# Kernel optimization log

Hardware: AMD Instinct MI355X
Metric: run time of the kernel (lower is better)

Reference implementation:

```python
import jax, jax.numpy as jnp
import numpy as np

N = 50000
DIN, DH, DOUT = 128, 128, 64
DEPTH = 3
TEMP = 1.0
WEIGHT = 0.5
LN_EPS = 1e-5
E_RAND = 1_600_000


def setup_inputs() -> dict:
    key = jax.random.key(0)
    ks = jax.random.split(key, 16)
    x = jax.random.normal(ks[0], (N, DIN), jnp.float32)
    # random edges + ring (guarantees degree >= 2 after symmetrization)
    src = jax.random.randint(ks[1], (E_RAND,), 0, N)
    dst = jax.random.randint(ks[2], (E_RAND,), 0, N)
    ring = jnp.arange(N)
    s = jnp.concatenate([src, ring])
    d = jnp.concatenate([dst, (ring + 1) % N])
    edge_index = jnp.stack([jnp.concatenate([s, d]), jnp.concatenate([d, s])]).astype(jnp.int64)  # [2, 3.3M], symmetric

    def glorot(k, i, o):
        return jax.random.normal(k, (i, o), jnp.float32) * jnp.sqrt(2.0 / (i + o)).astype(jnp.float32)

    return {
        "x": x, "edge_index": edge_index,
        "W0": glorot(ks[3], DIN, DH), "b0": jnp.zeros((DH,), jnp.float32),
        "W1": glorot(ks[4], DH, DH),  "b1": jnp.zeros((DH,), jnp.float32),
        "W2": glorot(ks[5], DH, DH),  "b2": jnp.zeros((DH,), jnp.float32),
        "W_out": glorot(ks[6], DH, DOUT), "b_out": jnp.zeros((DOUT,), jnp.float32),
        "gamma": jnp.ones((DH,), jnp.float32), "beta": jnp.zeros((DH,), jnp.float32),
    }


def _seg(vals, idx):
    return jax.ops.segment_sum(vals, idx, num_segments=N)


def _gcn_conv(h_in, W, b, src, dst):
    # PyG GCNConv: self-loops, sym norm D^-1/2 (A+I) D^-1/2
    h = h_in @ W
    ones = jnp.ones(src.shape, jnp.float32)
    deg = _seg(ones, dst) + 1.0  # degree incl. self-loop
    dinv = jax.lax.rsqrt(deg)
    msg = h[src] * (dinv[src] * dinv[dst])[:, None]
    return _seg(msg, dst) + h * (1.0 / deg)[:, None] + b


def _layernorm(x, g, b):
    m = jnp.mean(x, axis=-1, keepdims=True)
    v = jnp.mean((x - m) ** 2, axis=-1, keepdims=True)
    return (x - m) * jax.lax.rsqrt(v + LN_EPS) * g + b


def reference(x, edge_index, W0, b0, W1, b1, W2, b2, W_out, b_out, gamma, beta):
    src, dst = edge_index[0], edge_index[1]
    h = x
    for W, b in ((W0, b0), (W1, b1), (W2, b2)):
        h = _layernorm(jax.nn.relu(_gcn_conv(h, W, b, src, dst)), gamma, beta)
    emb = _gcn_conv(h, W_out, b_out, src, dst)  # [N, DOUT]

    # --- entropy gradient (edge-list form of the dense-A einsums) ---
    ones = jnp.ones(src.shape, jnp.float32)
    deg_adj = _seg(ones, src)                     # row sums of A (no self-loops)
    en_norm = 1.0 / jnp.sqrt(deg_adj * DH)        # uses hidden_dim, as in the original

    rn2 = jnp.sum(emb * emb, axis=1)              # ||X_i||^2
    dot = jnp.sum(emb[src] * emb[dst], axis=1)    # <X_i, X_j> per edge
    res1 = deg_adj * rn2
    res2 = _seg(dot, src)
    res3 = _seg(rn2[dst], src)
    energies = 0.5 * (res1 - 2.0 * res2 + res3) * en_norm  # normalize_energies=True

    logits = -energies / TEMP
    P = jax.nn.softmax(logits, axis=0) + 1e-10
    logP = jnp.log(P)
    S = -jnp.sum(P * logP)
    Pbar = P * (S + logP)                         # [N]

    nsumX = _seg(emb[dst], src)                   # sum_j A_ij X_j
    nsumP = _seg(Pbar[dst], src)                  # sum_j A_ij Pbar_j
    XP = emb * Pbar[:, None]
    g1 = deg_adj[:, None] * XP
    g2 = emb * nsumP[:, None]
    g3 = Pbar[:, None] * nsumX
    g4 = _seg(XP[dst], src)
    grad_S = (g1 + g2 - g3 - g4) / TEMP * en_norm[:, None]

    return emb + WEIGHT * grad_S
```

## Files before the change

### kernel.cpp

```cpp
#include <hip/hip_runtime.h>
#include <hip/hip_fp16.h>

#define DIN 128
#define DH  128
#define DFO 64
#define LN_EPS 1e-5f
#define WEIGHT 0.5f

#define MAXB  104
#define CAPB  48
#define FLUSH 32
#define SENT  0xFFFFFFFFu

typedef unsigned int uint32;
typedef unsigned short ushort16;

__device__ __forceinline__ float h_lo(uint32 u) { return __half2float(__ushort_as_half((unsigned short)(u & 0xFFFFu))); }
__device__ __forceinline__ float h_hi(uint32 u) { return __half2float(__ushort_as_half((unsigned short)(u >> 16))); }
__device__ __forceinline__ uint32 pack_h2(float a, float b) {
  return (uint32)__half_as_ushort(__float2half_rn(a)) | ((uint32)__half_as_ushort(__float2half_rn(b)) << 16);
}
__device__ __forceinline__ float ub0(uint32 u) { return (float)(u & 0xffu); }
__device__ __forceinline__ float ub1(uint32 u) { return (float)((u >> 8) & 0xffu); }
__device__ __forceinline__ float ub2(uint32 u) { return (float)((u >> 16) & 0xffu); }
__device__ __forceinline__ float ub3(uint32 u) { return (float)(u >> 24); }

__device__ __forceinline__ float wave_sum(float v) {
  #pragma unroll
  for (int off = 32; off > 0; off >>= 1) v += __shfl_xor(v, off);
  return v;
}
__device__ __forceinline__ float wave_max(float v) {
  #pragma unroll
  for (int off = 32; off > 0; off >>= 1) v = fmaxf(v, __shfl_xor(v, off));
  return v;
}

__device__ __forceinline__ void fq16u(float* a, uint4 u, float w) {
  a[0]  = fmaf(ub0(u.x), w, a[0]);  a[1]  = fmaf(ub1(u.x), w, a[1]);
  a[2]  = fmaf(ub2(u.x), w, a[2]);  a[3]  = fmaf(ub3(u.x), w, a[3]);
  a[4]  = fmaf(ub0(u.y), w, a[4]);  a[5]  = fmaf(ub1(u.y), w, a[5]);
  a[6]  = fmaf(ub2(u.y), w, a[6]);  a[7]  = fmaf(ub3(u.y), w, a[7]);
  a[8]  = fmaf(ub0(u.z), w, a[8]);  a[9]  = fmaf(ub1(u.z), w, a[9]);
  a[10] = fmaf(ub2(u.z), w, a[10]); a[11] = fmaf(ub3(u.z), w, a[11]);
  a[12] = fmaf(ub0(u.w), w, a[12]); a[13] = fmaf(ub1(u.w), w, a[13]);
  a[14] = fmaf(ub2(u.w), w, a[14]); a[15] = fmaf(ub3(u.w), w, a[15]);
}

__global__ __launch_bounds__(64) void k_prep(const float* __restrict__ g, const float* __restrict__ b,
                      const float* __restrict__ W1, const float* __restrict__ W2,
                      const float* __restrict__ Wo, float* __restrict__ Wg1,
                      float* __restrict__ Wg2, float* __restrict__ Wgo,
                      float* __restrict__ vecs) {
  int c = blockIdx.x * 64 + threadIdx.x;
  const float* W; float* Wg; float* gv; float* bv; int ld; int col;
  if (c < 128)      { W = W1; Wg = Wg1; gv = vecs;       bv = vecs + 128; ld = 128; col = c; }
  else if (c < 256) { W = W2; Wg = Wg2; gv = vecs + 256; bv = vecs + 384; ld = 128; col = c - 128; }
  else              { W = Wo; Wg = Wgo; gv = vecs + 512; bv = vecs + 576; ld = 64;  col = c - 256; }
  float gs = 0.f, bs = 0.f;
  for (int k = 0; k < 128; ++k) {
    float w = W[k * ld + col];
    float gk = g[k];
    Wg[k * ld + col] = gk * w;
    gs += gk * w;
    bs += b[k] * w;
  }
  gv[col] = gs; bv[col] = bs;
}

__global__ __launch_bounds__(256) void k_bin3(const int* __restrict__ src, const int* __restrict__ dst,
                       int E2, int nbc, int GCAP, int* __restrict__ gbcnt,
                       uint32* __restrict__ gpairs) {
  __shared__ uint32 lbuf[MAXB][CAPB];
  __shared__ int lcnt[MAXB];
  __shared__ int fbase[MAXB];
  __shared__ int fm[MAXB];
  __shared__ short flist[MAXB];
  __shared__ int fn;
  int wv = threadIdx.x >> 6, ln = threadIdx.x & 63;
  for (int b = threadIdx.x; b < nbc; b += 256) lcnt[b] = 0;
  __syncthreads();

  for (int base = blockIdx.x * 256; base < E2; base += gridDim.x * 256) {
    int i = base + threadIdx.x;
    if (i < E2) {
      int s = src[i], d = dst[i];
      int b0 = s >> 9;
      uint32 v0 = ((uint32)(s & 511) << 16) | (uint32)d;
      int sl = atomicAdd(&lcnt[b0], 1);
      if (sl < CAPB) lbuf[b0][sl] = v0;
      else { int g = atomicAdd(&gbcnt[b0 * 16], 1); gpairs[(size_t)b0 * GCAP + g] = v0; }
      int b1 = d >> 9;
      uint32 v1 = ((uint32)(d & 511) << 16) | (uint32)s;
      sl = atomicAdd(&lcnt[b1], 1);
      if (sl < CAPB) lbuf[b1][sl] = v1;
      else { int g = atomicAdd(&gbcnt[b1 * 16], 1); gpairs[(size_t)b1 * GCAP + g] = v1; }
    }
    if (threadIdx.x == 0) fn = 0;
    __syncthreads();
    if (threadIdx.x < nbc) {
      int m = lcnt[threadIdx.x];
      if (m >= FLUSH) {
        if (m > CAPB) m = CAPB;
        int r = (m + 15) & ~15;
        fbase[threadIdx.x] = atomicAdd(&gbcnt[threadIdx.x * 16], r);
        fm[threadIdx.x] = m;
        int fi = atomicAdd(&fn, 1);
        flist[fi] = (short)threadIdx.x;
      }
    }
    __syncthreads();
    int nf = fn;
    for (int fi = wv; fi < nf; fi += 4) {
      int b = flist[fi];
      int m = fm[b], r = (m + 15) & ~15, g = fbase[b];
      if (ln < r)
        gpairs[(size_t)b * GCAP + g + ln] = (ln < m) ? lbuf[b][ln] : SENT;
    }
    __syncthreads();
    if (threadIdx.x < nbc && lcnt[threadIdx.x] >= FLUSH) lcnt[threadIdx.x] = 0;
    __syncthreads();
  }
  if (threadIdx.x < nbc) {
    int m = lcnt[threadIdx.x]; if (m > CAPB) m = CAPB;
    fm[threadIdx.x] = m;
    if (m > 0) {
      int r = (m + 15) & ~15;
      fbase[threadIdx.x] = atomicAdd(&gbcnt[threadIdx.x * 16], r);
    }
  }
  __syncthreads();
  for (int b = wv; b < nbc; b += 4) {
    int m = fm[b];
    if (m > 0) {
      int r = (m + 15) & ~15, g = fbase[b];
      if (ln < r)
        gpairs[(size_t)b * GCAP + g + ln] = (ln < m) ? lbuf[b][ln] : SENT;
    }
  }
}

__global__ __launch_bounds__(1024) void k_csr(const uint32* __restrict__ gpairs, const int* __restrict__ gbcnt,
                      int GCAP, int GCAPC, int N, int* __restrict__ rowbeg, int* __restrict__ rowcnt,
                      float* __restrict__ dinv, float* __restrict__ cntf, ushort16* __restrict__ col) {
  __shared__ int hist[512];
  __shared__ int pos[512];
  int b = blockIdx.x, tid = threadIdx.x;
  if (tid < 512) hist[tid] = 0;
  __syncthreads();
  int m = gbcnt[b * 16];
  const uint32* pp = gpairs + (size_t)b * GCAP;
  for (int t = tid; t < m; t += 1024) {
    uint32 v = pp[t];
    if (v != SENT) atomicAdd(&hist[v >> 16], 1);
  }
  __syncthreads();
  int cnt = (tid < 512) ? hist[tid] : 0;
  for (int off = 1; off < 512; off <<= 1) {
    int u = (tid >= off && tid < 512) ? hist[tid - off] : 0;
    __syncthreads();
    if (tid < 512) hist[tid] += u;
    __syncthreads();
  }
  int cbase = b * GCAPC;
  if (tid < 512) {
    int excl = hist[tid] - cnt;
    pos[tid] = excl;
    int node = (b << 9) + tid;
    if (node < N) {
      rowbeg[node] = cbase + excl;
      rowcnt[node] = cnt;
      cntf[node] = (float)cnt;
      dinv[node] = rsqrtf((float)cnt + 1.0f);
    }
  }
  __syncthreads();
  for (int t = tid; t < m; t += 1024) {
    uint32 v = pp[t];
    if (v != SENT) {
      int sl = atomicAdd(&pos[v >> 16], 1);
      col[cbase + sl] = (ushort16)(v & 0xFFFFu);
    }
  }
}

template <int COLS, int MODE>
__global__ __launch_bounds__(256) void k_gemm(const void* __restrict__ Ap, const float* __restrict__ W,
                            const float* __restrict__ dinv, const float2* __restrict__ stats,
                            const float* __restrict__ gW, const float* __restrict__ bW,
                            uint32* __restrict__ qout, float* __restrict__ qsc, int N) {
  const int CG  = COLS / 4;
  const int RG  = 256 / CG;
  const int RPT = 64 / RG;
  __shared__ float4 At4[64 * 32];
  int t = threadIdx.x;
  int rbase = blockIdx.x * 64;
  #pragma unroll
  for (int i2 = 0; i2 < 8; ++i2) {
    int idx = t + 256 * i2;
    int row = idx >> 5, c4i = idx & 31;
    int gr = rbase + row;
    float4 v = make_float4(0.f, 0.f, 0.f, 0.f);
    if (gr < N) {
      if (MODE == 1) {
        uint2 p = ((const uint2*)Ap)[(size_t)gr * 32 + c4i];
        v = make_float4(h_lo(p.x), h_hi(p.x), h_lo(p.y), h_hi(p.y));
      } else {
        v = ((const float4*)Ap)[(size_t)gr * 32 + c4i];
      }
    }
    At4[idx] = v;
  }
  __syncthreads();
  int c4 = t % CG, rg = t / CG;
  float acc[RPT][4];
  #pragma unroll
  for (int r = 0; r < RPT; ++r) { acc[r][0] = acc[r][1] = acc[r][2] = acc[r][3] = 0.f; }
  const float4* W4 = (const float4*)W;
  #pragma unroll 2
  for (int k4 = 0; k4 < 32; ++k4) {
    float4 w0 = W4[(k4 * 4 + 0) * CG + c4];
    float4 w1 = W4[(k4 * 4 + 1) * CG + c4];
    float4 w2 = W4[(k4 * 4 + 2) * CG + c4];
    float4 w3 = W4[(k4 * 4 + 3) * CG + c4];
    #pragma unroll
    for (int r = 0; r < RPT; ++r) {
      float4 av = At4[(rg * RPT + r) * 32 + k4];
      acc[r][0] = fmaf(av.x, w0.x, acc[r][0]); acc[r][0] = fmaf(av.y, w1.x, acc[r][0]);
      acc[r][0] = fmaf(av.z, w2.x, acc[r][0]); acc[r][0] = fmaf(av.w, w3.x, acc[r][0]);
      acc[r][1] = fmaf(av.x, w0.y, acc[r][1]); acc[r][1] = fmaf(av.y, w1.y, acc[r][1]);
      acc[r][1] = fmaf(av.z, w2.y, acc[r][1]); acc[r][1] = fmaf(av.w, w3.y, acc[r][1]);
      acc[r][2] = fmaf(av.x, w0.z, acc[r][2]); acc[r][2] = fmaf(av.y, w1.z, acc[r][2]);
      acc[r][2] = fmaf(av.z, w2.z, acc[r][2]); acc[r][2] = fmaf(av.w, w3.z, acc[r][2]);
      acc[r][3] = fmaf(av.x, w0.w, acc[r][3]); acc[r][3] = fmaf(av.y, w1.w, acc[r][3]);
      acc[r][3] = fmaf(av.z, w2.w, acc[r][3]); acc[r][3] = fmaf(av.w, w3.w, acc[r][3]);
    }
  }
  float4 g4 = make_float4(0.f, 0.f, 0.f, 0.f), b4 = make_float4(0.f, 0.f, 0.f, 0.f);
  if (MODE == 1) { g4 = ((const float4*)gW)[c4]; b4 = ((const float4*)bW)[c4]; }
  #pragma unroll
  for (int r = 0; r < RPT; ++r) {
    int gr = rbase + rg * RPT + r;
    float o0 = 0.f, o1 = 0.f, o2 = 0.f, o3 = 0.f;
    if (gr < N) {
      float s = dinv[gr];
      if (MODE == 1) {
        float2 st = stats[gr];
        o0 = s * (st.y * (acc[r][0] - st.x * g4.x) + b4.x);
        o1 = s * (st.y * (acc[r][1] - st.x * g4.y) + b4.y);
        o2 = s * (st.y * (acc[r][2] - st.x * g4.z) + b4.z);
        o3 = s * (st.y * (acc[r][3] - st.x * g4.w) + b4.w);
      } else {
        o0 = acc[r][0] * s; o1 = acc[r][1] * s; o2 = acc[r][2] * s; o3 = acc[r][3] * s;
      }
    }
    float mx = fmaxf(fmaxf(fabsf(o0), fabsf(o1)), fmaxf(fabsf(o2), fabsf(o3)));
    #pragma unroll
    for (int m = 1; m < CG; m <<= 1) mx = fmaxf(mx, __shfl_xor(mx, m));
    if (gr < N) {
      float inv = (mx > 0.f) ? 127.f / mx : 0.f;
      int q0 = (int)rintf(o0 * inv) + 128, q1 = (int)rintf(o1 * inv) + 128;
      int q2 = (int)rintf(o2 * inv) + 128, q3 = (int)rintf(o3 * inv) + 128;
      uint32 qw = (uint32)q0 | ((uint32)q1 << 8) | ((uint32)q2 << 16) | ((uint32)q3 << 24);
      qout[(size_t)gr * CG + c4] = qw;
      if (c4 == 0) qsc[gr] = mx * (1.f / 127.f);
    }
  }
}

__global__ __launch_bounds__(64) void k_aggh(const uint4* __restrict__ hq4, const float* __restrict__ hsc,
                      const int* __restrict__ rowbeg, const int* __restrict__ rowcnt,
                      const ushort16* __restrict__ col, const float* __restrict__ dinv,
                      const float* __restrict__ bias, uint4* __restrict__ vh4,
                      float2* __restrict__ stats, int N) {
  int i = blockIdx.x, lane = threadIdx.x;
  int f = lane & 7, sl = lane >> 3;
  int beg = rowbeg[i], end = beg + rowcnt[i];
  float a[16];
  #pragma unroll
  for (int k = 0; k < 16; ++k) a[k] = 0.f;
  float ssum = 0.f;
  {
    float si = hsc[i];
    if (lane < 8) fq16u(a, hq4[(size_t)i * 8 + f], si);
    if (lane == 0) ssum += si;
  }
  int t = beg + sl;
  for (; t + 8 < end; t += 16) {
    int j0 = col[t], j1 = col[t + 8];
    float s0 = hsc[j0], s1 = hsc[j1];
    uint4 u0 = hq4[(size_t)j0 * 8 + f];
    uint4 u1 = hq4[(size_t)j1 * 8 + f];
    fq16u(a, u0, s0); fq16u(a, u1, s1);
    if (f == 0) ssum += s0 + s1;
  }
  if (t < end) {
    int j = col[t];
    float s0 = hsc[j];
    fq16u(a, hq4[(size_t)j * 8 + f], s0);
    if (f == 0) ssum += s0;
  }
  #pragma unroll
  for (int k = 0; k < 16; ++k) {
    a[k] += __shfl_xor(a[k], 8);
    a[k] += __shfl_xor(a[k], 16);
    a[k] += __shfl_xor(a[k], 32);
  }
  float ssT = wave_sum(ssum) * 128.f;
  if (lane < 8) {
    float di = dinv[i];
    const float4* bb = (const float4*)bias + f * 4;
    float s = 0.f, s2 = 0.f;
    #pragma unroll
    for (int q = 0; q < 4; ++q) {
      float4 b4 = bb[q];
      float v0 = fmaxf(fmaf(a[q*4+0] - ssT, di, b4.x), 0.f);
      float v1 = fmaxf(fmaf(a[q*4+1] - ssT, di, b4.y), 0.f);
      float v2 = fmaxf(fmaf(a[q*4+2] - ssT, di, b4.z), 0.f);
      float v3 = fmaxf(fmaf(a[q*4+3] - ssT, di, b4.w), 0.f);
      a[q*4+0] = v0; a[q*4+1] = v1; a[q*4+2] = v2; a[q*4+3] = v3;
      s += (v0 + v1) + (v2 + v3);
      s2 += (v0*v0 + v1*v1) + (v2*v2 + v3*v3);
    }
    s += __shfl_xor(s, 1); s2 += __shfl_xor(s2, 1);
    s += __shfl_xor(s, 2); s2 += __shfl_xor(s2, 2);
    s += __shfl_xor(s, 4); s2 += __shfl_xor(s2, 4);
    uint4 o0, o1;
    o0.x = pack_h2(a[0], a[1]);   o0.y = pack_h2(a[2], a[3]);
    o0.z = pack_h2(a[4], a[5]);   o0.w = pack_h2(a[6], a[7]);
    o1.x = pack_h2(a[8], a[9]);   o1.y = pack_h2(a[10], a[11]);
    o1.z = pack_h2(a[12], a[13]); o1.w = pack_h2(a[14], a[15]);
    vh4[(size_t)i * 16 + f * 2]     = o0;
    vh4[(size_t)i * 16 + f * 2 + 1] = o1;
    if (lane == 0) {
      float mean = s * (1.f / 128.f);
      float var  = s2 * (1.f / 128.f) - mean * mean;
      stats[i] = make_float2(mean, rsqrtf(var + LN_EPS));
    }
  }
}

__global__ __launch_bounds__(64) void k_agg_out(const uint4* __restrict__ hq4, const float* __restrict__ hsc,
                          const int* __restrict__ rowbeg, const int* __restrict__ rowcnt,
                          const ushort16* __restrict__ col, const float* __restrict__ dinv,
                          const float* __restrict__ bias, float* __restrict__ embf,
                          uint4* __restrict__ embq4, float2* __restrict__ escr2, int N) {
  int i = blockIdx.x, lane = threadIdx.x;
  int f4 = lane & 3, sl = lane >> 2;
  int beg = rowbeg[i], end = beg + rowcnt[i];
  float a[16];
  #pragma unroll
  for (int k = 0; k < 16; ++k) a[k] = 0.f;
  float ssum = 0.f;
  {
    float si = hsc[i];
    if (lane < 4) fq16u(a, hq4[(size_t)i * 4 + f4], si);
    if (lane == 0) ssum += si;
  }
  int t = beg + sl;
  for (; t + 16 < end; t += 32) {
    int j0 = col[t], j1 = col[t + 16];
    float s0 = hsc[j0], s1 = hsc[j1];
    uint4 u0 = hq4[(size_t)j0 * 4 + f4];
    uint4 u1 = hq4[(size_t)j1 * 4 + f4];
    fq16u(a, u0, s0); fq16u(a, u1, s1);
    if (f4 == 0) ssum += s0 + s1;
  }
  if (t < end) {
    int j = col[t];
    float s0 = hsc[j];
    fq16u(a, hq4[(size_t)j * 4 + f4], s0);
    if (f4 == 0) ssum += s0;
  }
  #pragma unroll
  for (int k = 0; k < 16; ++k) {
    a[k] += __shfl_xor(a[k], 4);  a[k] += __shfl_xor(a[k], 8);
    a[k] += __shfl_xor(a[k], 16); a[k] += __shfl_xor(a[k], 32);
  }
  float ssT = wave_sum(ssum) * 128.f;
  if (lane < 4) {
    float di = dinv[i];
    const float4* bb = (const float4*)bias + f4 * 4;
    float s2 = 0.f, mx = 0.f;
    #pragma unroll
    for (int q = 0; q < 4; ++q) {
      float4 b4 = bb[q];
      float e0 = fmaf(a[q*4+0] - ssT, di, b4.x);
      float e1 = fmaf(a[q*4+1] - ssT, di, b4.y);
      float e2 = fmaf(a[q*4+2] - ssT, di, b4.z);
      float e3 = fmaf(a[q*4+3] - ssT, di, b4.w);
      a[q*4+0] = e0; a[q*4+1] = e1; a[q*4+2] = e2; a[q*4+3] = e3;
      s2 += (e0*e0 + e1*e1) + (e2*e2 + e3*e3);
      mx = fmaxf(mx, fmaxf(fmaxf(fabsf(e0), fabsf(e1)), fmaxf(fabsf(e2), fabsf(e3))));
      ((float4*)embf)[(size_t)i * 16 + f4 * 4 + q] = make_float4(e0, e1, e2, e3);
    }
    s2 += __shfl_xor(s2, 1); s2 += __shfl_xor(s2, 2);
    mx = fmaxf(mx, __shfl_xor(mx, 1)); mx = fmaxf(mx, __shfl_xor(mx, 2));
    float inv = (mx > 0.f) ? 127.f / mx : 0.f;
    uint4 qo;
    uint32* qw = (uint32*)&qo;
    #pragma unroll
    for (int q = 0; q < 4; ++q) {
      int q0 = (int)rintf(a[q*4+0] * inv) + 128, q1 = (int)rintf(a[q*4+1] * inv) + 128;
      int q2 = (int)rintf(a[q*4+2] * inv) + 128, q3 = (int)rintf(a[q*4+3] * inv) + 128;
      qw[q] = (uint32)q0 | ((uint32)q1 << 8) | ((uint32)q2 << 16) | ((uint32)q3 << 24);
    }
    embq4[(size_t)i * 4 + f4] = qo;
    if (lane == 0) escr2[i] = make_float2(mx * (1.f / 127.f), s2);
  }
}

__global__ __launch_bounds__(64) void k_passA(const float* __restrict__ embf, const uint4* __restrict__ embq4,
                        const float2* __restrict__ escr2, const int* __restrict__ rowbeg,
                        const int* __restrict__ rowcnt, const ushort16* __restrict__ col,
                        const float* __restrict__ cntf, float* __restrict__ nsumX,
                        float* __restrict__ logits, int N) {
  int i = blockIdx.x, lane = threadIdx.x;
  int f4 = lane & 3, sl = lane >> 2;
  int beg = rowbeg[i], end = beg + rowcnt[i];
  float a[16];
  #pragma unroll
  for (int k = 0; k < 16; ++k) a[k] = 0.f;
  float r3 = 0.f, escs = 0.f;
  int t = beg + sl;
  for (; t + 16 < end; t += 32) {
    int j0 = col[t], j1 = col[t + 16];
    float2 er0 = escr2[j0], er1 = escr2[j1];
    uint4 u0 = embq4[(size_t)j0 * 4 + f4];
    uint4 u1 = embq4[(size_t)j1 * 4 + f4];
    fq16u(a, u0, er0.x); fq16u(a, u1, er1.x);
    if (f4 == 0) { r3 += er0.y + er1.y; escs += er0.x + er1.x; }
  }
  if (t < end) {
    int j = col[t];
    float2 er = escr2[j];
    fq16u(a, embq4[(size_t)j * 4 + f4], er.x);
    if (f4 == 0) { r3 += er.y; escs += er.x; }
  }
  #pragma unroll
  for (int k = 0; k < 16; ++k) {
    a[k] += __shfl_xor(a[k], 4);  a[k] += __shfl_xor(a[k], 8);
    a[k] += __shfl_xor(a[k], 16); a[k] += __shfl_xor(a[k], 32);
  }
  r3 = wave_sum(r3);
  float ssT = wave_sum(escs) * 128.f;
  if (lane < 4) {
    float dd = 0.f;
    #pragma unroll
    for (int q = 0; q < 4; ++q) {
      float n0 = a[q*4+0] - ssT, n1 = a[q*4+1] - ssT;
      float n2 = a[q*4+2] - ssT, n3 = a[q*4+3] - ssT;
      float4 e = ((const float4*)embf)[(size_t)i * 16 + f4 * 4 + q];
      dd += e.x * n0 + e.y * n1 + e.z * n2 + e.w * n3;
      ((float4*)nsumX)[(size_t)i * 16 + f4 * 4 + q] = make_float4(n0, n1, n2, n3);
    }
    dd += __shfl_xor(dd, 1); dd += __shfl_xor(dd, 2);
    if (lane == 0) {
      float c = cntf[i];
      float en = rsqrtf(c * 128.0f);
      logits[i] = -0.5f * (c * escr2[i].y - 2.f * dd + r3) * en;
    }
  }
}

__global__ __launch_bounds__(256) void k_sm1(const float* __restrict__ logits, int N,
                                             float4* __restrict__ partials) {
  int idx = blockIdx.x * 256 + threadIdx.x;
  int w = threadIdx.x >> 6, ln = threadIdx.x & 63;
  float x = (idx < N) ? logits[idx] : -3.4e38f;
  float m = wave_max(x);
  __shared__ float red[3][4];
  if (ln == 0) red[0][w] = m;
  __syncthreads();
  float M = fmaxf(fmaxf(red[0][0], red[0][1]), fmaxf(red[0][2], red[0][3]));
  float ev = (idx < N) ? expf(x - M) : 0.f;
  float tv = (idx < N) ? (x - M) * ev : 0.f;
  float se = wave_sum(ev), st = wave_sum(tv);
  if (ln == 0) { red[1][w] = se; red[2][w] = st; }
  __syncthreads();
  if (threadIdx.x == 0)
    partials[blockIdx.x] = make_float4(M, red[1][0] + red[1][1] + red[1][2] + red[1][3],
                                          red[2][0] + red[2][1] + red[2][2] + red[2][3], 0.f);
}

__global__ __launch_bounds__(256) void k_sm2(const float4* __restrict__ partials, int nb,
                                             float* __restrict__ scal) {
  int tid = threadIdx.x;
  int w = tid >> 6, ln = tid & 63;
  float4 p = (tid < nb) ? partials[tid] : make_float4(-3.4e38f, 0.f, 0.f, 0.f);
  float m = wave_max(p.x);
  __shared__ float red[3][4];
  if (ln == 0) red[0][w] = m;
  __syncthreads();
  float M = fmaxf(fmaxf(red[0][0], red[0][1]), fmaxf(red[0][2], red[0][3]));
  float sc = (tid < nb) ? expf(p.x - M) : 0.f;
  float se = p.y * sc;
  float tt = (p.z + (p.x - M) * p.y) * sc;
  se = wave_sum(se); tt = wave_sum(tt);
  if (ln == 0) { red[1][w] = se; red[2][w] = tt; }
  __syncthreads();
  if (tid == 0) {
    float SE = red[1][0] + red[1][1] + red[1][2] + red[1][3];
    float TT = red[2][0] + red[2][1] + red[2][2] + red[2][3];
    scal[0] = M;
    scal[1] = SE;
    scal[2] = logf(SE) - TT / SE;
  }
}

__global__ __launch_bounds__(256) void k_pbar(const float* __restrict__ logits, int N,
                     const float* __restrict__ scal, const float2* __restrict__ escr2,
                     float2* __restrict__ pw2) {
  float M = scal[0], SE = scal[1], S = scal[2];
  int i = blockIdx.x * blockDim.x + threadIdx.x;
  int stride = gridDim.x * blockDim.x;
  for (; i < N; i += stride) {
    float p = expf(logits[i] - M) / SE + 1e-10f;
    float pb = p * (S + logf(p));
    pw2[i] = make_float2(pb, pb * escr2[i].x);
  }
}

__global__ __launch_bounds__(64) void k_passB(const float* __restrict__ embf, const uint4* __restrict__ embq4,
                        const float2* __restrict__ pw2, const int* __restrict__ rowbeg,
                        const int* __restrict__ rowcnt, const ushort16* __restrict__ col,
                        const float* __restrict__ cntf, float* __restrict__ outp, int N) {
  int i = blockIdx.x, lane = threadIdx.x;
  int f4 = lane & 3, sl = lane >> 2;
  int beg = rowbeg[i], end = beg + rowcnt[i];
  float a[16];
  #pragma unroll
  for (int k = 0; k < 16; ++k) a[k] = 0.f;
  float sp = 0.f, pys = 0.f;
  int t = beg + sl;
  for (; t + 16 < end; t += 32) {
    int j0 = col[t], j1 = col[t + 16];
    float2 p0 = pw2[j0], p1 = pw2[j1];
    uint4 u0 = embq4[(size_t)j0 * 4 + f4];
    uint4 u1 = embq4[(size_t)j1 * 4 + f4];
    fq16u(a, u0, p0.y); fq16u(a, u1, p1.y);
    if (f4 == 0) { sp += p0.x + p1.x; pys += p0.y + p1.y; }
  }
  if (t < end) {
    int j = col[t];
    float2 p = pw2[j];
    fq16u(a, embq4[(size_t)j * 4 + f4], p.y);
    if (f4 == 0) { sp += p.x; pys += p.y; }
  }
  #pragma unroll
  for (int k = 0; k < 16; ++k) {
    a[k] += __shfl_xor(a[k], 4);  a[k] += __shfl_xor(a[k], 8);
    a[k] += __shfl_xor(a[k], 16); a[k] += __shfl_xor(a[k], 32);
  }
  sp = wave_sum(sp);
  float ssT = wave_sum(pys) * 128.f;
  if (lane < 4) {
    float Pi = pw2[i].x;
    float c = cntf[i];
    float wgt = WEIGHT * rsqrtf(c * 128.0f);
    #pragma unroll
    for (int q = 0; q < 4; ++q) {
      float4 e = ((const float4*)embf)[(size_t)i * 16 + f4 * 4 + q];
      float4 n = ((const float4*)outp)[(size_t)i * 16 + f4 * 4 + q];
      float x0 = a[q*4+0] - ssT, x1 = a[q*4+1] - ssT;
      float x2 = a[q*4+2] - ssT, x3 = a[q*4+3] - ssT;
      float g0 = c * e.x * Pi + e.x * sp - Pi * n.x - x0;
      float g1 = c * e.y * Pi + e.y * sp - Pi * n.y - x1;
      float g2 = c * e.z * Pi + e.z * sp - Pi * n.z - x2;
      float g3 = c * e.w * Pi + e.w * sp - Pi * n.w - x3;
      ((float4*)outp)[(size_t)i * 16 + f4 * 4 + q] =
          make_float4(fmaf(wgt, g0, e.x), fmaf(wgt, g1, e.y), fmaf(wgt, g2, e.z), fmaf(wgt, g3, e.w));
    }
  }
}

extern "C" void kernel_launch(void* const* d_in, const int* in_sizes, int n_in,
                              void* d_out, int out_size, void* d_ws, size_t ws_size,
                              hipStream_t stream) {
  const float* x     = (const float*)d_in[0];
  const int*   ei    = (const int*)d_in[1];
  const float* W0    = (const float*)d_in[2];
  const float* b0    = (const float*)d_in[3];
  const float* W1    = (const float*)d_in[4];
  const float* b1    = (const float*)d_in[5];
  const float* W2    = (const float*)d_in[6];
  const float* b2    = (const float*)d_in[7];
  const float* Wo    = (const float*)d_in[8];
  const float* bo    = (const float*)d_in[9];
  const float* gamma = (const float*)d_in[10];
  const float* beta  = (const float*)d_in[11];

  int N = in_sizes[0] / DIN;
  int E = in_sizes[1] / 2;
  int E2 = E / 2;
  const int* src = ei;
  const int* dst = ei + E;
  int nbc = (N + 511) >> 9;
  int perb = E / nbc;
  int GCAP  = ((perb + perb / 3 + 8192) + 15) & ~15;
  int GCAPC = perb + 4096;

  char* w = (char*)d_ws;
  auto alloc = [&](size_t bytes) { void* p = w; w += (bytes + 255) & ~(size_t)255; return p; };
  char* regA = (char*)alloc((size_t)N * 128 * 2);
  char* regB = (char*)alloc((size_t)N * 128);
  char* pad  = (char*)alloc((size_t)3 * 1024 * 1024);
  (void)pad;
  ushort16* colx = (ushort16*)alloc((size_t)nbc * GCAPC * 2);
  int*    rowbeg = (int*)alloc((size_t)N * 4);
  int*    rowcnt = (int*)alloc((size_t)N * 4);
  float*  dinv   = (float*)alloc((size_t)N * 4);
  float*  cntf   = (float*)alloc((size_t)N * 4);
  float*  logits = (float*)alloc((size_t)N * 4);
  float*  hsc    = (float*)alloc((size_t)N * 4);
  float*  oscq   = (float*)alloc((size_t)N * 4);
  float2* escr2  = (float2*)alloc((size_t)N * 8);
  float2* pw2    = (float2*)alloc((size_t)N * 8);
  float2* stats  = (float2*)alloc((size_t)N * 8);
  float*  Wg1    = (float*)alloc(128 * 128 * 4);
  float*  Wg2    = (float*)alloc(128 * 128 * 4);
  float*  Wgo    = (float*)alloc(128 * 64 * 4);
  float*  vecs   = (float*)alloc(640 * 4);
  int*    gbcnt  = (int*)alloc((size_t)MAXB * 16 * 4);
  float4* partials = (float4*)alloc(4096);
  float*  scal   = (float*)alloc(256);

  uint32* gpairs = (uint32*)regA;
  uint4*  vh4    = (uint4*)regA;
  float*  embf   = (float*)regA;
  uint32* hq     = (uint32*)regB;
  uint32* hoq    = (uint32*)regB;
  uint4*  embq4  = (uint4*)(regB + (size_t)N * 64);

  hipMemsetAsync(gbcnt, 0, (size_t)MAXB * 64, stream);
  k_prep<<<5, 64, 0, stream>>>(gamma, beta, W1, W2, Wo, Wg1, Wg2, Wgo, vecs);
  k_bin3<<<1024, 256, 0, stream>>>(src, dst, E2, nbc, GCAP, gbcnt, gpairs);
  k_csr<<<nbc, 1024, 0, stream>>>(gpairs, gbcnt, GCAP, GCAPC, N, rowbeg, rowcnt, dinv, cntf, colx);

  int gblk = (N + 63) / 64;

  k_gemm<DH, 0><<<gblk, 256, 0, stream>>>(x, W0, dinv, nullptr, nullptr, nullptr, hq, hsc, N);
  k_aggh<<<N, 64, 0, stream>>>((const uint4*)hq, hsc, rowbeg, rowcnt, colx, dinv, b0, vh4, stats, N);
  k_gemm<DH, 1><<<gblk, 256, 0, stream>>>(vh4, Wg1, dinv, stats, vecs, vecs + 128, hq, hsc, N);
  k_aggh<<<N, 64, 0, stream>>>((const uint4*)hq, hsc, rowbeg, rowcnt, colx, dinv, b1, vh4, stats, N);
  k_gemm<DH, 1><<<gblk, 256, 0, stream>>>(vh4, Wg2, dinv, stats, vecs + 256, vecs + 384, hq, hsc, N);
  k_aggh<<<N, 64, 0, stream>>>((const uint4*)hq, hsc, rowbeg, rowcnt, colx, dinv, b2, vh4, stats, N);
  k_gemm<DFO, 1><<<gblk, 256, 0, stream>>>(vh4, Wgo, dinv, stats, vecs + 512, vecs + 576, hoq, oscq, N);
  k_agg_out<<<N, 64, 0, stream>>>((const uint4*)hoq, oscq, rowbeg, rowcnt, colx, dinv, bo, embf, embq4, escr2, N);

  k_passA<<<N, 64, 0, stream>>>(embf, embq4, escr2, rowbeg, rowcnt, colx, cntf, (float*)d_out, logits, N);
  int nb = (N + 255) / 256;
  k_sm1<<<nb, 256, 0, stream>>>(logits, N, partials);
  k_sm2<<<1, 256, 0, stream>>>(partials, nb, scal);
  k_pbar<<<256, 256, 0, stream>>>(logits, N, scal, escr2, pw2);
  k_passB<<<N, 64, 0, stream>>>(embf, embq4, pw2, rowbeg, rowcnt, colx, cntf, (float*)d_out, N);
}
```

Baseline: 568.8 us.

## Switch to global-scale int8 quantization with packed integer accumulation in aggregations

Replaces per-row int8 quantization scales with one global scale per tensor. The GEMMs now write fp16 output, track the tensor max with an atomic, and separate k_qh/k_qf kernels quantize with that scale. This lets the gather-aggregation kernels sum packed bytes as SWAR 16-bit integer lanes instead of per-element float FMAs, and it drops the per-neighbor scale loads. The cost is extra quantize passes with fp16 round-trip traffic, coarser precision for rows with small magnitude, and a dependence on degree staying small enough that the 16-bit lane sums do not overflow.

```diff
diff --git a/kernel.cpp b/kernel.cpp
--- a/kernel.cpp
+++ b/kernel.cpp
@@ -11,6 +11,7 @@
 #define CAPB  48
 #define FLUSH 32
 #define SENT  0xFFFFFFFFu
+#define BMASK 0x00FF00FFu
 
 typedef unsigned int uint32;
 typedef unsigned short ushort16;
@@ -46,6 +47,28 @@
   a[12] = fmaf(ub0(u.w), w, a[12]); a[13] = fmaf(ub1(u.w), w, a[13]);
   a[14] = fmaf(ub2(u.w), w, a[14]); a[15] = fmaf(ub3(u.w), w, a[15]);
 }
+
+#define ACCINT(u) do { \
+  ae0 += (u).x & BMASK; ao0 += ((u).x >> 8) & BMASK; \
+  ae1 += (u).y & BMASK; ao1 += ((u).y >> 8) & BMASK; \
+  ae2 += (u).z & BMASK; ao2 += ((u).z >> 8) & BMASK; \
+  ae3 += (u).w & BMASK; ao3 += ((u).w >> 8) & BMASK; } while (0)
+
+#define REDINT(off) do { \
+  ae0 += __shfl_xor(ae0, off); ao0 += __shfl_xor(ao0, off); \
+  ae1 += __shfl_xor(ae1, off); ao1 += __shfl_xor(ao1, off); \
+  ae2 += __shfl_xor(ae2, off); ao2 += __shfl_xor(ao2, off); \
+  ae3 += __shfl_xor(ae3, off); ao3 += __shfl_xor(ao3, off); } while (0)
+
+#define UNPACK16(a) do { \
+  a[0]  = (float)(ae0 & 0xFFFFu); a[2]  = (float)(ae0 >> 16); \
+  a[1]  = (float)(ao0 & 0xFFFFu); a[3]  = (float)(ao0 >> 16); \
+  a[4]  = (float)(ae1 & 0xFFFFu); a[6]  = (float)(ae1 >> 16); \
+  a[5]  = (float)(ao1 & 0xFFFFu); a[7]  = (float)(ao1 >> 16); \
+  a[8]  = (float)(ae2 & 0xFFFFu); a[10] = (float)(ae2 >> 16); \
+  a[9]  = (float)(ao2 & 0xFFFFu); a[11] = (float)(ao2 >> 16); \
+  a[12] = (float)(ae3 & 0xFFFFu); a[14] = (float)(ae3 >> 16); \
+  a[13] = (float)(ao3 & 0xFFFFu); a[15] = (float)(ao3 >> 16); } while (0)
 
 __global__ __launch_bounds__(64) void k_prep(const float* __restrict__ g, const float* __restrict__ b,
                       const float* __restrict__ W1, const float* __restrict__ W2,
@@ -188,7 +211,7 @@
 __global__ __launch_bounds__(256) void k_gemm(const void* __restrict__ Ap, const float* __restrict__ W,
                             const float* __restrict__ dinv, const float2* __restrict__ stats,
                             const float* __restrict__ gW, const float* __restrict__ bW,
-                            uint32* __restrict__ qout, float* __restrict__ qsc, int N) {
+                            uint2* __restrict__ out16, float* __restrict__ gmx, int slot, int N) {
   const int CG  = COLS / 4;
   const int RG  = 256 / CG;
   const int RPT = 64 / RG;
@@ -238,12 +261,13 @@
   }
   float4 g4 = make_float4(0.f, 0.f, 0.f, 0.f), b4 = make_float4(0.f, 0.f, 0.f, 0.f);
   if (MODE == 1) { g4 = ((const float4*)gW)[c4]; b4 = ((const float4*)bW)[c4]; }
+  float mxt = 0.f;
   #pragma unroll
   for (int r = 0; r < RPT; ++r) {
     int gr = rbase + rg * RPT + r;
-    float o0 = 0.f, o1 = 0.f, o2 = 0.f, o3 = 0.f;
     if (gr < N) {
       float s = dinv[gr];
+      float o0, o1, o2, o3;
       if (MODE == 1) {
         float2 st = stats[gr];
         o0 = s * (st.y * (acc[r][0] - st.x * g4.x) + b4.x);
@@ -253,71 +277,89 @@
       } else {
         o0 = acc[r][0] * s; o1 = acc[r][1] * s; o2 = acc[r][2] * s; o3 = acc[r][3] * s;
       }
-    }
-    float mx = fmaxf(fmaxf(fabsf(o0), fabsf(o1)), fmaxf(fabsf(o2), fabsf(o3)));
-    #pragma unroll
-    for (int m = 1; m < CG; m <<= 1) mx = fmaxf(mx, __shfl_xor(mx, m));
-    if (gr < N) {
-      float inv = (mx > 0.f) ? 127.f / mx : 0.f;
-      int q0 = (int)rintf(o0 * inv) + 128, q1 = (int)rintf(o1 * inv) + 128;
-      int q2 = (int)rintf(o2 * inv) + 128, q3 = (int)rintf(o3 * inv) + 128;
-      uint32 qw = (uint32)q0 | ((uint32)q1 << 8) | ((uint32)q2 << 16) | ((uint32)q3 << 24);
-      qout[(size_t)gr * CG + c4] = qw;
-      if (c4 == 0) qsc[gr] = mx * (1.f / 127.f);
-    }
-  }
-}
-
-__global__ __launch_bounds__(64) void k_aggh(const uint4* __restrict__ hq4, const float* __restrict__ hsc,
+      mxt = fmaxf(mxt, fmaxf(fmaxf(fabsf(o0), fabsf(o1)), fmaxf(fabsf(o2), fabsf(o3))));
+      uint2 o;
+      o.x = pack_h2(o0, o1);
+      o.y = pack_h2(o2, o3);
+      out16[(size_t)gr * CG + c4] = o;
+    }
+  }
+  mxt = wave_max(mxt);
+  if ((t & 63) == 0) atomicMax((unsigned*)&gmx[slot], __float_as_uint(mxt));
+}
+
+__global__ __launch_bounds__(256) void k_qh(const uint4* __restrict__ src, uint2* __restrict__ dst,
+                                            const float* __restrict__ gmx, int slot, int total) {
+  float g = gmx[slot];
+  float inv = (g > 0.f) ? 127.f / g : 0.f;
+  int i = blockIdx.x * 256 + threadIdx.x;
+  for (; i < total; i += gridDim.x * 256) {
+    uint4 u = src[i];
+    int q0 = (int)rintf(h_lo(u.x) * inv) + 128, q1 = (int)rintf(h_hi(u.x) * inv) + 128;
+    int q2 = (int)rintf(h_lo(u.y) * inv) + 128, q3 = (int)rintf(h_hi(u.y) * inv) + 128;
+    int q4 = (int)rintf(h_lo(u.z) * inv) + 128, q5 = (int)rintf(h_hi(u.z) * inv) + 128;
+    int q6 = (int)rintf(h_lo(u.w) * inv) + 128, q7 = (int)rintf(h_hi(u.w) * inv) + 128;
+    uint2 o;
+    o.x = (uint32)q0 | ((uint32)q1 << 8) | ((uint32)q2 << 16) | ((uint32)q3 << 24);
+    o.y = (uint32)q4 | ((uint32)q5 << 8) | ((uint32)q6 << 16) | ((uint32)q7 << 24);
+    dst[i] = o;
+  }
+}
+
+__global__ __launch_bounds__(256) void k_qf(const float4* __restrict__ src, uint2* __restrict__ dst,
+                                            const float* __restrict__ gmx, int slot, int total) {
+  float g = gmx[slot];
+  float inv = (g > 0.f) ? 127.f / g : 0.f;
+  int i = blockIdx.x * 256 + threadIdx.x;
+  for (; i < total; i += gridDim.x * 256) {
+    float4 a = src[2 * i], b = src[2 * i + 1];
+    int q0 = (int)rintf(a.x * inv) + 128, q1 = (int)rintf(a.y * inv) + 128;
+    int q2 = (int)rintf(a.z * inv) + 128, q3 = (int)rintf(a.w * inv) + 128;
+    int q4 = (int)rintf(b.x * inv) + 128, q5 = (int)rintf(b.y * inv) + 128;
+    int q6 = (int)rintf(b.z * inv) + 128, q7 = (int)rintf(b.w * inv) + 128;
+    uint2 o;
+    o.x = (uint32)q0 | ((uint32)q1 << 8) | ((uint32)q2 << 16) | ((uint32)q3 << 24);
+    o.y = (uint32)q4 | ((uint32)q5 << 8) | ((uint32)q6 << 16) | ((uint32)q7 << 24);
+    dst[i] = o;
+  }
+}
+
+__global__ __launch_bounds__(64) void k_aggh(const uint4* __restrict__ hq4, const float* __restrict__ gmx, int slot,
                       const int* __restrict__ rowbeg, const int* __restrict__ rowcnt,
                       const ushort16* __restrict__ col, const float* __restrict__ dinv,
-                      const float* __restrict__ bias, uint4* __restrict__ vh4,
-                      float2* __restrict__ stats, int N) {
+                      const float* __restrict__ cntf, const float* __restrict__ bias,
+                      uint4* __restrict__ vh4, float2* __restrict__ stats, int N) {
   int i = blockIdx.x, lane = threadIdx.x;
   int f = lane & 7, sl = lane >> 3;
   int beg = rowbeg[i], end = beg + rowcnt[i];
-  float a[16];
-  #pragma unroll
-  for (int k = 0; k < 16; ++k) a[k] = 0.f;
-  float ssum = 0.f;
-  {
-    float si = hsc[i];
-    if (lane < 8) fq16u(a, hq4[(size_t)i * 8 + f], si);
-    if (lane == 0) ssum += si;
-  }
+  uint32 ae0 = 0, ao0 = 0, ae1 = 0, ao1 = 0, ae2 = 0, ao2 = 0, ae3 = 0, ao3 = 0;
+  if (lane < 8) { uint4 u = hq4[(size_t)i * 8 + f]; ACCINT(u); }
   int t = beg + sl;
   for (; t + 8 < end; t += 16) {
     int j0 = col[t], j1 = col[t + 8];
-    float s0 = hsc[j0], s1 = hsc[j1];
     uint4 u0 = hq4[(size_t)j0 * 8 + f];
     uint4 u1 = hq4[(size_t)j1 * 8 + f];
-    fq16u(a, u0, s0); fq16u(a, u1, s1);
-    if (f == 0) ssum += s0 + s1;
-  }
-  if (t < end) {
-    int j = col[t];
-    float s0 = hsc[j];
-    fq16u(a, hq4[(size_t)j * 8 + f], s0);
-    if (f == 0) ssum += s0;
-  }
-  #pragma unroll
-  for (int k = 0; k < 16; ++k) {
-    a[k] += __shfl_xor(a[k], 8);
-    a[k] += __shfl_xor(a[k], 16);
-    a[k] += __shfl_xor(a[k], 32);
-  }
-  float ssT = wave_sum(ssum) * 128.f;
+    ACCINT(u0); ACCINT(u1);
+  }
+  if (t < end) { uint4 u = hq4[(size_t)col[t] * 8 + f]; ACCINT(u); }
+  REDINT(8); REDINT(16); REDINT(32);
   if (lane < 8) {
+    float gs = gmx[slot] * (1.f / 127.f);
+    float cntT = cntf[i] + 1.0f;
+    float base = 128.f * cntT;
     float di = dinv[i];
+    float w = gs * di;
+    float a[16];
+    UNPACK16(a);
     const float4* bb = (const float4*)bias + f * 4;
     float s = 0.f, s2 = 0.f;
     #pragma unroll
     for (int q = 0; q < 4; ++q) {
       float4 b4 = bb[q];
-      float v0 = fmaxf(fmaf(a[q*4+0] - ssT, di, b4.x), 0.f);
-      float v1 = fmaxf(fmaf(a[q*4+1] - ssT, di, b4.y), 0.f);
-      float v2 = fmaxf(fmaf(a[q*4+2] - ssT, di, b4.z), 0.f);
-      float v3 = fmaxf(fmaf(a[q*4+3] - ssT, di, b4.w), 0.f);
+      float v0 = fmaxf(fmaf(a[q*4+0] - base, w, b4.x), 0.f);
+      float v1 = fmaxf(fmaf(a[q*4+1] - base, w, b4.y), 0.f);
+      float v2 = fmaxf(fmaf(a[q*4+2] - base, w, b4.z), 0.f);
+      float v3 = fmaxf(fmaf(a[q*4+3] - base, w, b4.w), 0.f);
       a[q*4+0] = v0; a[q*4+1] = v1; a[q*4+2] = v2; a[q*4+3] = v3;
       s += (v0 + v1) + (v2 + v3);
       s2 += (v0*v0 + v1*v1) + (v2*v2 + v3*v3);
@@ -340,125 +382,102 @@
   }
 }
 
-__global__ __launch_bounds__(64) void k_agg_out(const uint4* __restrict__ hq4, const float* __restrict__ hsc,
+__global__ __launch_bounds__(64) void k_agg_out(const uint4* __restrict__ hq4, const float* __restrict__ gmx, int slot,
                           const int* __restrict__ rowbeg, const int* __restrict__ rowcnt,
                           const ushort16* __restrict__ col, const float* __restrict__ dinv,
-                          const float* __restrict__ bias, float* __restrict__ embf,
-                          uint4* __restrict__ embq4, float2* __restrict__ escr2, int N) {
+                          const float* __restrict__ cntf, const float* __restrict__ bias,
+                          float* __restrict__ embf, float* __restrict__ rn2,
+                          float* __restrict__ gmxout, int oslot, int N) {
   int i = blockIdx.x, lane = threadIdx.x;
   int f4 = lane & 3, sl = lane >> 2;
   int beg = rowbeg[i], end = beg + rowcnt[i];
-  float a[16];
-  #pragma unroll
-  for (int k = 0; k < 16; ++k) a[k] = 0.f;
-  float ssum = 0.f;
-  {
-    float si = hsc[i];
-    if (lane < 4) fq16u(a, hq4[(size_t)i * 4 + f4], si);
-    if (lane == 0) ssum += si;
-  }
+  uint32 ae0 = 0, ao0 = 0, ae1 = 0, ao1 = 0, ae2 = 0, ao2 = 0, ae3 = 0, ao3 = 0;
+  if (lane < 4) { uint4 u = hq4[(size_t)i * 4 + f4]; ACCINT(u); }
   int t = beg + sl;
   for (; t + 16 < end; t += 32) {
     int j0 = col[t], j1 = col[t + 16];
-    float s0 = hsc[j0], s1 = hsc[j1];
     uint4 u0 = hq4[(size_t)j0 * 4 + f4];
     uint4 u1 = hq4[(size_t)j1 * 4 + f4];
-    fq16u(a, u0, s0); fq16u(a, u1, s1);
-    if (f4 == 0) ssum += s0 + s1;
-  }
-  if (t < end) {
-    int j = col[t];
-    float s0 = hsc[j];
-    fq16u(a, hq4[(size_t)j * 4 + f4], s0);
-    if (f4 == 0) ssum += s0;
-  }
-  #pragma unroll
-  for (int k = 0; k < 16; ++k) {
-    a[k] += __shfl_xor(a[k], 4);  a[k] += __shfl_xor(a[k], 8);
-    a[k] += __shfl_xor(a[k], 16); a[k] += __shfl_xor(a[k], 32);
-  }
-  float ssT = wave_sum(ssum) * 128.f;
+    ACCINT(u0); ACCINT(u1);
+  }
+  if (t < end) { uint4 u = hq4[(size_t)col[t] * 4 + f4]; ACCINT(u); }
+  REDINT(4); REDINT(8); REDINT(16); REDINT(32);
+  float mx = 0.f;
   if (lane < 4) {
+    float gs = gmx[slot] * (1.f / 127.f);
+    float cntT = cntf[i] + 1.0f;
+    float base = 128.f * cntT;
     float di = dinv[i];
+    float w = gs * di;
+    float a[16];
+    UNPACK16(a);
     const float4* bb = (const float4*)bias + f4 * 4;
-    float s2 = 0.f, mx = 0.f;
+    float s2 = 0.f;
     #pragma unroll
     for (int q = 0; q < 4; ++q) {
       float4 b4 = bb[q];
-      float e0 = fmaf(a[q*4+0] - ssT, di, b4.x);
-      float e1 = fmaf(a[q*4+1] - ssT, di, b4.y);
-      float e2 = fmaf(a[q*4+2] - ssT, di, b4.z);
-      float e3 = fmaf(a[q*4+3] - ssT, di, b4.w);
-      a[q*4+0] = e0; a[q*4+1] = e1; a[q*4+2] = e2; a[q*4+3] = e3;
+      float e0 = fmaf(a[q*4+0] - base, w, b4.x);
+      float e1 = fmaf(a[q*4+1] - base, w, b4.y);
+      float e2 = fmaf(a[q*4+2] - base, w, b4.z);
+      float e3 = fmaf(a[q*4+3] - base, w, b4.w);
       s2 += (e0*e0 + e1*e1) + (e2*e2 + e3*e3);
       mx = fmaxf(mx, fmaxf(fmaxf(fabsf(e0), fabsf(e1)), fmaxf(fabsf(e2), fabsf(e3))));
       ((float4*)embf)[(size_t)i * 16 + f4 * 4 + q] = make_float4(e0, e1, e2, e3);
     }
     s2 += __shfl_xor(s2, 1); s2 += __shfl_xor(s2, 2);
     mx = fmaxf(mx, __shfl_xor(mx, 1)); mx = fmaxf(mx, __shfl_xor(mx, 2));
-    float inv = (mx > 0.f) ? 127.f / mx : 0.f;
-    uint4 qo;
-    uint32* qw = (uint32*)&qo;
-    #pragma unroll
-    for (int q = 0; q < 4; ++q) {
-      int q0 = (int)rintf(a[q*4+0] * inv) + 128, q1 = (int)rintf(a[q*4+1] * inv) + 128;
-      int q2 = (int)rintf(a[q*4+2] * inv) + 128, q3 = (int)rintf(a[q*4+3] * inv) + 128;
-      qw[q] = (uint32)q0 | ((uint32)q1 << 8) | ((uint32)q2 << 16) | ((uint32)q3 << 24);
-    }
-    embq4[(size_t)i * 4 + f4] = qo;
-    if (lane == 0) escr2[i] = make_float2(mx * (1.f / 127.f), s2);
+    if (lane == 0) {
+      rn2[i] = s2;
+      atomicMax((unsigned*)&gmxout[oslot], __float_as_uint(mx));
+    }
   }
 }
 
 __global__ __launch_bounds__(64) void k_passA(const float* __restrict__ embf, const uint4* __restrict__ embq4,
-                        const float2* __restrict__ escr2, const int* __restrict__ rowbeg,
-                        const int* __restrict__ rowcnt, const ushort16* __restrict__ col,
-                        const float* __restrict__ cntf, float* __restrict__ nsumX,
-                        float* __restrict__ logits, int N) {
+                        const float* __restrict__ gmx, int slot, const float* __restrict__ rn2,
+                        const int* __restrict__ rowbeg, const int* __restrict__ rowcnt,
+                        const ushort16* __restrict__ col, const float* __restrict__ cntf,
+                        float* __restrict__ nsumX, float* __restrict__ logits, int N) {
   int i = blockIdx.x, lane = threadIdx.x;
   int f4 = lane & 3, sl = lane >> 2;
   int beg = rowbeg[i], end = beg + rowcnt[i];
-  float a[16];
-  #pragma unroll
-  for (int k = 0; k < 16; ++k) a[k] = 0.f;
-  float r3 = 0.f, escs = 0.f;
+  uint32 ae0 = 0, ao0 = 0, ae1 = 0, ao1 = 0, ae2 = 0, ao2 = 0, ae3 = 0, ao3 = 0;
+  float r3 = 0.f;
   int t = beg + sl;
   for (; t + 16 < end; t += 32) {
     int j0 = col[t], j1 = col[t + 16];
-    float2 er0 = escr2[j0], er1 = escr2[j1];
     uint4 u0 = embq4[(size_t)j0 * 4 + f4];
     uint4 u1 = embq4[(size_t)j1 * 4 + f4];
-    fq16u(a, u0, er0.x); fq16u(a, u1, er1.x);
-    if (f4 == 0) { r3 += er0.y + er1.y; escs += er0.x + er1.x; }
+    ACCINT(u0); ACCINT(u1);
+    if (f4 == 0) r3 += rn2[j0] + rn2[j1];
   }
   if (t < end) {
     int j = col[t];
-    float2 er = escr2[j];
-    fq16u(a, embq4[(size_t)j * 4 + f4], er.x);
-    if (f4 == 0) { r3 += er.y; escs += er.x; }
-  }
-  #pragma unroll
-  for (int k = 0; k < 16; ++k) {
-    a[k] += __shfl_xor(a[k], 4);  a[k] += __shfl_xor(a[k], 8);
-    a[k] += __shfl_xor(a[k], 16); a[k] += __shfl_xor(a[k], 32);
-  }
+    uint4 u = embq4[(size_t)j * 4 + f4];
+    ACCINT(u);
+    if (f4 == 0) r3 += rn2[j];
+  }
+  REDINT(4); REDINT(8); REDINT(16); REDINT(32);
   r3 = wave_sum(r3);
-  float ssT = wave_sum(escs) * 128.f;
   if (lane < 4) {
+    float gs = gmx[slot] * (1.f / 127.f);
+    float deg = cntf[i];
+    float base = 128.f * deg;
+    float a[16];
+    UNPACK16(a);
     float dd = 0.f;
     #pragma unroll
     for (int q = 0; q < 4; ++q) {
-      float n0 = a[q*4+0] - ssT, n1 = a[q*4+1] - ssT;
-      float n2 = a[q*4+2] - ssT, n3 = a[q*4+3] - ssT;
+      float n0 = (a[q*4+0] - base) * gs, n1 = (a[q*4+1] - base) * gs;
+      float n2 = (a[q*4+2] - base) * gs, n3 = (a[q*4+3] - base) * gs;
       float4 e = ((const float4*)embf)[(size_t)i * 16 + f4 * 4 + q];
       dd += e.x * n0 + e.y * n1 + e.z * n2 + e.w * n3;
       ((float4*)nsumX)[(size_t)i * 16 + f4 * 4 + q] = make_float4(n0, n1, n2, n3);
     }
     dd += __shfl_xor(dd, 1); dd += __shfl_xor(dd, 2);
     if (lane == 0) {
-      float c = cntf[i];
-      float en = rsqrtf(c * 128.0f);
-      logits[i] = -0.5f * (c * escr2[i].y - 2.f * dd + r3) * en;
+      float en = rsqrtf(deg * 128.0f);
+      logits[i] = -0.5f * (deg * rn2[i] - 2.f * dd + r3) * en;
     }
   }
 }
@@ -509,15 +528,16 @@
 }
 
 __global__ __launch_bounds__(256) void k_pbar(const float* __restrict__ logits, int N,
-                     const float* __restrict__ scal, const float2* __restrict__ escr2,
+                     const float* __restrict__ scal, const float* __restrict__ gmx, int slot,
                      float2* __restrict__ pw2) {
   float M = scal[0], SE = scal[1], S = scal[2];
+  float gs = gmx[slot] * (1.f / 127.f);
   int i = blockIdx.x * blockDim.x + threadIdx.x;
   int stride = gridDim.x * blockDim.x;
   for (; i < N; i += stride) {
     float p = expf(logits[i] - M) / SE + 1e-10f;
     float pb = p * (S + logf(p));
-    pw2[i] = make_float2(pb, pb * escr2[i].x);
+    pw2[i] = make_float2(pb, pb * gs);
   }
 }
 
@@ -603,18 +623,15 @@
   char* w = (char*)d_ws;
   auto alloc = [&](size_t bytes) { void* p = w; w += (bytes + 255) & ~(size_t)255; return p; };
   char* regA = (char*)alloc((size_t)N * 128 * 2);
+  char* regC = (char*)alloc((size_t)N * 128 * 2);
   char* regB = (char*)alloc((size_t)N * 128);
-  char* pad  = (char*)alloc((size_t)3 * 1024 * 1024);
-  (void)pad;
   ushort16* colx = (ushort16*)alloc((size_t)nbc * GCAPC * 2);
   int*    rowbeg = (int*)alloc((size_t)N * 4);
   int*    rowcnt = (int*)alloc((size_t)N * 4);
   float*  dinv   = (float*)alloc((size_t)N * 4);
   float*  cntf   = (float*)alloc((size_t)N * 4);
+  float*  rn2    = (float*)alloc((size_t)N * 4);
   float*  logits = (float*)alloc((size_t)N * 4);
-  float*  hsc    = (float*)alloc((size_t)N * 4);
-  float*  oscq   = (float*)alloc((size_t)N * 4);
-  float2* escr2  = (float2*)alloc((size_t)N * 8);
   float2* pw2    = (float2*)alloc((size_t)N * 8);
   float2* stats  = (float2*)alloc((size_t)N * 8);
   float*  Wg1    = (float*)alloc(128 * 128 * 4);
@@ -624,34 +641,45 @@
   int*    gbcnt  = (int*)alloc((size_t)MAXB * 16 * 4);
   float4* partials = (float4*)alloc(4096);
   float*  scal   = (float*)alloc(256);
+  float*  gmx    = (float*)alloc(256);
 
   uint32* gpairs = (uint32*)regA;
   uint4*  vh4    = (uint4*)regA;
   float*  embf   = (float*)regA;
+  uint2*  hsf    = (uint2*)regC;
   uint32* hq     = (uint32*)regB;
   uint32* hoq    = (uint32*)regB;
   uint4*  embq4  = (uint4*)(regB + (size_t)N * 64);
 
   hipMemsetAsync(gbcnt, 0, (size_t)MAXB * 64, stream);
+  hipMemsetAsync(gmx, 0, 64, stream);
   k_prep<<<5, 64, 0, stream>>>(gamma, beta, W1, W2, Wo, Wg1, Wg2, Wgo, vecs);
   k_bin3<<<1024, 256, 0, stream>>>(src, dst, E2, nbc, GCAP, gbcnt, gpairs);
   k_csr<<<nbc, 1024, 0, stream>>>(gpairs, gbcnt, GCAP, GCAPC, N, rowbeg, rowcnt, dinv, cntf, colx);
 
   int gblk = (N + 63) / 64;
-
-  k_gemm<DH, 0><<<gblk, 256, 0, stream>>>(x, W0, dinv, nullptr, nullptr, nullptr, hq, hsc, N);
-  k_aggh<<<N, 64, 0, stream>>>((const uint4*)hq, hsc, rowbeg, rowcnt, colx, dinv, b0, vh4, stats, N);
-  k_gemm<DH, 1><<<gblk, 256, 0, stream>>>(vh4, Wg1, dinv, stats, vecs, vecs + 128, hq, hsc, N);
-  k_aggh<<<N, 64, 0, stream>>>((const uint4*)hq, hsc, rowbeg, rowcnt, colx, dinv, b1, vh4, stats, N);
-  k_gemm<DH, 1><<<gblk, 256, 0, stream>>>(vh4, Wg2, dinv, stats, vecs + 256, vecs + 384, hq, hsc, N);
-  k_aggh<<<N, 64, 0, stream>>>((const uint4*)hq, hsc, rowbeg, rowcnt, colx, dinv, b2, vh4, stats, N);
-  k_gemm<DFO, 1><<<gblk, 256, 0, stream>>>(vh4, Wgo, dinv, stats, vecs + 512, vecs + 576, hoq, oscq, N);
-  k_agg_out<<<N, 64, 0, stream>>>((const uint4*)hoq, oscq, rowbeg, rowcnt, colx, dinv, bo, embf, embq4, escr2, N);
-
-  k_passA<<<N, 64, 0, stream>>>(embf, embq4, escr2, rowbeg, rowcnt, colx, cntf, (float*)d_out, logits, N);
+  int qtotH = N * 16;
+  int qtotO = N * 8;
+
+  k_gemm<DH, 0><<<gblk, 256, 0, stream>>>(x, W0, dinv, nullptr, nullptr, nullptr, hsf, gmx, 0, N);
+  k_qh<<<1024, 256, 0, stream>>>((const uint4*)hsf, (uint2*)hq, gmx, 0, qtotH);
+  k_aggh<<<N, 64, 0, stream>>>((const uint4*)hq, gmx, 0, rowbeg, rowcnt, colx, dinv, cntf, b0, vh4, stats, N);
+  k_gemm<DH, 1><<<gblk, 256, 0, stream>>>(vh4, Wg1, dinv, stats, vecs, vecs + 128, hsf, gmx, 1, N);
+  k_qh<<<1024, 256, 0, stream>>>((const uint4*)hsf, (uint2*)hq, gmx, 1, qtotH);
+  k_aggh<<<N, 64, 0, stream>>>((const uint4*)hq, gmx, 1, rowbeg, rowcnt, colx, dinv, cntf, b1, vh4, stats, N);
+  k_gemm<DH, 1><<<gblk, 256, 0, stream>>>(vh4, Wg2, dinv, stats, vecs + 256, vecs + 384, hsf, gmx, 2, N);
+  k_qh<<<1024, 256, 0, stream>>>((const uint4*)hsf, (uint2*)hq, gmx, 2, qtotH);
+  k_aggh<<<N, 64, 0, stream>>>((const uint4*)hq, gmx, 2, rowbeg, rowcnt, colx, dinv, cntf, b2, vh4, stats, N);
+  k_gemm<DFO, 1><<<gblk, 256, 0, stream>>>(vh4, Wgo, dinv, stats, vecs + 512, vecs + 576, hsf, gmx, 3, N);
+  k_qh<<<1024, 256, 0, stream>>>((const uint4*)hsf, (uint2*)hoq, gmx, 3, qtotO);
+  k_agg_out<<<N, 64, 0, stream>>>((const uint4*)hoq, gmx, 3, rowbeg, rowcnt, colx, dinv, cntf, bo,
+                                  embf, rn2, gmx, 4, N);
+  k_qf<<<1024, 256, 0, stream>>>((const float4*)embf, (uint2*)embq4, gmx, 4, qtotO);
+
+  k_passA<<<N, 64, 0, stream>>>(embf, embq4, gmx, 4, rn2, rowbeg, rowcnt, colx, cntf, (float*)d_out, logits, N);
   int nb = (N + 255) / 256;
   k_sm1<<<nb, 256, 0, stream>>>(logits, N, partials);
   k_sm2<<<1, 256, 0, stream>>>(partials, nb, scal);
-  k_pbar<<<256, 256, 0, stream>>>(logits, N, scal, escr2, pw2);
+  k_pbar<<<256, 256, 0, stream>>>(logits, N, scal, gmx, 4, pw2);
   k_passB<<<N, 64, 0, stream>>>(embf, embq4, pw2, rowbeg, rowcnt, colx, cntf, (float*)d_out, N);
 }
```

New measurement: 1.217 ms. +113.9%, slower.
